# Performance work log

Hardware: AMD Instinct MI355X
Metric: run time of the kernel (lower is better)

The kernel has to match this reference:

```python
import jax, jax.numpy as jnp
import numpy as np

D_MODEL = 1024
PATCH = 16
HID = 256
VOCAB = 256

def setup_inputs() -> dict:
    key = jax.random.key(0)
    ks = jax.random.split(key, 12)
    B, N = 16, 512
    s = lambda *sh: 1.0 / np.sqrt(sh[-1])
    inp = {
        'latents': jax.random.normal(ks[0], (B, N, D_MODEL), dtype=jnp.float32),
        'target_bytes': jax.random.randint(ks[1], (B, N * PATCH), 0, VOCAB, dtype=jnp.int64),
        'W_proj': jax.random.normal(ks[2], (HID, D_MODEL), dtype=jnp.float32) * s(HID, D_MODEL),
        'b_proj': jnp.zeros((HID,), dtype=jnp.float32),
        'emb_table': jax.random.normal(ks[3], (VOCAB, HID), dtype=jnp.float32),
        'W_ih': jax.random.normal(ks[4], (3 * HID, 2 * HID), dtype=jnp.float32) * s(1, 2 * HID),
        'W_hh': jax.random.normal(ks[5], (3 * HID, HID), dtype=jnp.float32) * s(1, HID),
        'b_ih': jnp.zeros((3 * HID,), dtype=jnp.float32),
        'b_hh': jnp.zeros((3 * HID,), dtype=jnp.float32),
        'W_head': jax.random.normal(ks[6], (VOCAB, HID), dtype=jnp.float32) * s(VOCAB, HID),
        'b_head': jnp.zeros((VOCAB,), dtype=jnp.float32),
    }
    return inp

def _gru_scan(x_proj, W_hh, b_hh, h0):
    # x_proj: [T, BN, 3H] precomputed input projections (incl. b_ih)
    def step(h, xg):
        hg = h @ W_hh.T + b_hh                      # [BN, 3H]
        xr, xz, xn = jnp.split(xg, 3, axis=-1)
        hr, hz, hn = jnp.split(hg, 3, axis=-1)
        r = jax.nn.sigmoid(xr + hr)
        z = jax.nn.sigmoid(xz + hz)
        n = jnp.tanh(xn + r * hn)
        h_new = (1.0 - z) * n + z * h
        return h_new, h_new
    _, outs = jax.lax.scan(step, h0, x_proj)
    return outs                                      # [T, BN, H]

def reference(latents, target_bytes, W_proj, b_proj, emb_table, W_ih, W_hh, b_ih, b_hh, W_head, b_head):
    B, N, D = latents.shape
    BN = B * N
    latent_ctx = (latents.reshape(BN, D) @ W_proj.T + b_proj)        # [BN, H]
    targets = target_bytes.reshape(BN, PATCH)
    sos = jnp.zeros((BN, 1), dtype=targets.dtype)
    rnn_in_bytes = jnp.concatenate([sos, targets[:, :-1]], axis=1)   # [BN, P]
    emb = emb_table[rnn_in_bytes]                                    # [BN, P, H]
    lat_exp = jnp.broadcast_to(latent_ctx[:, None, :], (BN, PATCH, HID))
    rnn_input = jnp.concatenate([emb, lat_exp], axis=-1)             # [BN, P, 2H]
    x_proj = jnp.einsum('bpi,gi->bpg', rnn_input, W_ih) + b_ih       # [BN, P, 3H]
    h0 = jnp.zeros((BN, HID), dtype=latents.dtype)
    outs = _gru_scan(jnp.swapaxes(x_proj, 0, 1), W_hh, b_hh, h0)     # [P, BN, H]
    outs = jnp.swapaxes(outs, 0, 1)                                  # [BN, P, H]
    logits = jnp.einsum('bph,vh->bpv', outs, W_head) + b_head        # [BN, P, 256]
    return logits.reshape(B, N, PATCH, VOCAB)
```

## Files before the change

kernel.cpp:

```cpp
#include <hip/hip_runtime.h>
#include <math.h>

#define NSEQ 8192
#define PATCHL 16
#define HIDN 256
#define VOCABN 256

typedef __attribute__((ext_vector_type(4))) float f32x4;
typedef __attribute__((ext_vector_type(8))) short bf16x8;

__device__ __forceinline__ unsigned short f2bf(float f) {
    unsigned int x = __float_as_uint(f);
    unsigned int r = (x + 0x7fffu + ((x >> 16) & 1u)) >> 16;
    return (unsigned short)r;
}
__device__ __forceinline__ float bf2f(unsigned short b) {
    return __uint_as_float(((unsigned int)b) << 16);
}
__device__ __forceinline__ float sigf(float x)   { return 1.f / (1.f + __expf(-x)); }
__device__ __forceinline__ float tanhf_(float x) { return 2.f / (1.f + __expf(-2.f * x)) - 1.f; }

__global__ __launch_bounds__(256)
void pack_frag(const float* __restrict__ src, int ld, int col0, int nks,
               unsigned short* __restrict__ dst)
{
    const int g = blockIdx.x * 256 + threadIdx.x;
    const int lane = g & 63;
    const int ks = (g / 64) % nks;
    const int T  = g / (64 * nks);
    const float* s = src + (size_t)(T * 16 + (lane & 15)) * ld + col0 + ks * 32 + ((lane >> 4) & 3) * 8;
    unsigned int q[4];
#pragma unroll
    for (int j = 0; j < 4; j++) {
        unsigned int lo = f2bf(s[2 * j]);
        unsigned int hi = f2bf(s[2 * j + 1]);
        q[j] = lo | (hi << 16);
    }
    uint4 v; v.x = q[0]; v.y = q[1]; v.z = q[2]; v.w = q[3];
    *(uint4*)(dst + (size_t)g * 8) = v;
}

template<bool ASRC_BF16, int OUT_MODE>
__global__ __launch_bounds__(512)
void gemm_mfma(const void* __restrict__ Asrc, int lda,
               const unsigned short* __restrict__ bpack, int nks_total,
               const float* __restrict__ bias, void* __restrict__ Cdst, int ldc,
               int K)
{
    const int tid = threadIdx.x;
    const int w = tid >> 6, lane = tid & 63;
    const int l15 = lane & 15, kg = (lane >> 4) & 3;
    const int bm = blockIdx.x * 128, bn = blockIdx.y * 64;

    __shared__ unsigned short As[2][128 * 64];

    const int srow = tid >> 2;
    const int scol = (tid & 3) * 16;
    const int nkt = K / 64;

    f32x4 acc[4];
#pragma unroll
    for (int nt = 0; nt < 4; nt++) acc[nt] = 0.f;

    const int wb0 = srow * 128 + ((scol * 2) ^ ((srow & 7) << 4));
    const int wb1 = srow * 128 + ((scol * 2 + 16) ^ ((srow & 7) << 4));

#define STAGE(kt, buf) do {                                                         \
        const int gk = (kt) * 64 + scol;                                            \
        unsigned short tmp[16];                                                     \
        if (ASRC_BF16) {                                                            \
            const unsigned short* A = (const unsigned short*)Asrc;                  \
            *(uint4*)(tmp)     = *(const uint4*)(A + (size_t)(bm + srow) * lda + gk);      \
            *(uint4*)(tmp + 8) = *(const uint4*)(A + (size_t)(bm + srow) * lda + gk + 8);  \
        } else {                                                                    \
            const float* A = (const float*)Asrc;                                    \
            const float4 a0 = *(const float4*)(A + (size_t)(bm + srow) * lda + gk);       \
            const float4 a1 = *(const float4*)(A + (size_t)(bm + srow) * lda + gk + 4);   \
            const float4 a2 = *(const float4*)(A + (size_t)(bm + srow) * lda + gk + 8);   \
            const float4 a3 = *(const float4*)(A + (size_t)(bm + srow) * lda + gk + 12);  \
            tmp[0] = f2bf(a0.x);  tmp[1] = f2bf(a0.y);  tmp[2] = f2bf(a0.z);  tmp[3] = f2bf(a0.w);   \
            tmp[4] = f2bf(a1.x);  tmp[5] = f2bf(a1.y);  tmp[6] = f2bf(a1.z);  tmp[7] = f2bf(a1.w);   \
            tmp[8] = f2bf(a2.x);  tmp[9] = f2bf(a2.y);  tmp[10] = f2bf(a2.z); tmp[11] = f2bf(a2.w);  \
            tmp[12] = f2bf(a3.x); tmp[13] = f2bf(a3.y); tmp[14] = f2bf(a3.z); tmp[15] = f2bf(a3.w);  \
        }                                                                           \
        *(uint4*)((char*)As[buf] + wb0) = *(uint4*)tmp;                             \
        *(uint4*)((char*)As[buf] + wb1) = *(uint4*)(tmp + 8);                       \
    } while (0)

    STAGE(0, 0);
    __syncthreads();

    for (int kt = 0; kt < nkt; ++kt) {
        if (kt + 1 < nkt) STAGE(kt + 1, (kt + 1) & 1);
        const unsigned short* buf = As[kt & 1];
        const int row = w * 16 + l15;
#pragma unroll
        for (int ks = 0; ks < 2; ++ks) {
            const int bo = row * 128 + (((ks * 64) + kg * 16) ^ ((row & 7) << 4));
            const bf16x8 a = *(const bf16x8*)((const char*)buf + bo);
#pragma unroll
            for (int nt = 0; nt < 4; ++nt) {
                const int T = blockIdx.y * 4 + nt;
                const bf16x8 b = *(const bf16x8*)(bpack + (((size_t)T * nks_total + (kt * 2 + ks)) * 64 + lane) * 8);
                acc[nt] = __builtin_amdgcn_mfma_f32_16x16x32_bf16(a, b, acc[nt], 0, 0, 0);
            }
        }
        __syncthreads();
    }
#undef STAGE

#pragma unroll
    for (int nt = 0; nt < 4; ++nt) {
        const int n = bn + nt * 16 + l15;
        const float bv = bias ? bias[n] : 0.f;
#pragma unroll
        for (int rr = 0; rr < 4; ++rr) {
            const int m = bm + w * 16 + kg * 4 + rr;
            const float v = acc[nt][rr] + bv;
            if (OUT_MODE == 0)      ((float*)Cdst)[(size_t)m * ldc + n] = v;
            else if (OUT_MODE == 1) ((unsigned short*)Cdst)[(size_t)m * ldc + n] = f2bf(v);
            else                    ((unsigned short*)Cdst)[(size_t)m * 1024 + (n & 255) * 4 + (n >> 8)] = f2bf(v);
        }
    }
}

#define G4S 1032
__global__ __launch_bounds__(512)
__attribute__((amdgpu_waves_per_eu(2, 2)))
void gru_scan_fused(const int* __restrict__ bytes,
                    const unsigned short* __restrict__ latg4,
                    const unsigned short* __restrict__ pmx4,
                    const unsigned short* __restrict__ wpack,
                    const float* __restrict__ b_hh,
                    unsigned short* __restrict__ hh,
                    int seq0)
{
    const int tid  = threadIdx.x;
    const int w    = tid >> 6;
    const int lane = tid & 63;
    const int l15  = lane & 15;
    const int kg   = (lane >> 4) & 3;
    const int s0l  = blockIdx.x * 32;
    const int s0g  = seq0 + s0l;

    __shared__ unsigned short PMs[32 * G4S];
    __shared__ unsigned short LG[32 * G4S];
    __shared__ unsigned short H[32 * 256];
    __shared__ int BYs[512];

    BYs[tid] = bytes[(size_t)s0g * PATCHL + tid];

#pragma unroll
    for (int j = 0; j < 8; ++j) {
        const int idx = j * 512 + tid;
        const int row = idx >> 7, col = idx & 127;
        *(uint4*)(LG + row * G4S + col * 8) =
            *(const uint4*)(latg4 + (size_t)(s0g + row) * 1024 + col * 8);
    }

    float bhr[2], bhz[2], bhn[2];
#pragma unroll
    for (int nt = 0; nt < 2; nt++) {
        const int u = w * 32 + nt * 16 + l15;
        bhr[nt] = b_hh[u]; bhz[nt] = b_hh[256 + u]; bhn[nt] = b_hh[512 + u];
    }

    float hreg[2][2][4];
#pragma unroll
    for (int mt = 0; mt < 2; mt++)
#pragma unroll
        for (int nt = 0; nt < 2; nt++)
#pragma unroll
            for (int rr = 0; rr < 4; rr++) hreg[mt][nt][rr] = 0.f;

    __syncthreads();

    for (int p = 0; p < PATCHL; ++p) {
#pragma unroll
        for (int j = 0; j < 8; ++j) {
            const int idx = j * 512 + tid;
            const int row = idx >> 7, col = idx & 127;
            const int bv = p ? BYs[row * PATCHL + p - 1] : 0;
            *(uint4*)(PMs + row * G4S + col * 8) =
                *(const uint4*)(pmx4 + (size_t)bv * 1024 + col * 8);
        }

        if (p) {
#pragma unroll
            for (int rj = 0; rj < 4; ++rj) {
                const int row = w * 4 + rj;
                const int boff = (lane * 8) ^ ((row & 7) << 4);
                const ushort4 v = *(const ushort4*)((const char*)(H + row * 256) + boff);
                *(ushort4*)(hh + ((size_t)(s0l + row) * PATCHL + (p - 1)) * 256 + lane * 4) = v;
            }
        }

        f32x4 accr[2][2], accz[2][2], accn[2][2];
#pragma unroll
        for (int mt = 0; mt < 2; mt++)
#pragma unroll
            for (int nt = 0; nt < 2; nt++) {
                accr[mt][nt] = 0.f; accz[mt][nt] = 0.f; accn[mt][nt] = 0.f;
            }
        if (p != 0) {
#pragma unroll
            for (int g = 0; g < 3; ++g)
#pragma unroll
                for (int nt = 0; nt < 2; ++nt) {
                    const int T = g * 16 + w * 2 + nt;
                    bf16x8 B[8];
#pragma unroll
                    for (int ks = 0; ks < 8; ++ks)
                        B[ks] = *(const bf16x8*)(wpack + (((size_t)T * 8 + ks) * 64 + lane) * 8);
#pragma unroll
                    for (int ks = 0; ks < 8; ++ks)
#pragma unroll
                        for (int mt = 0; mt < 2; ++mt) {
                            const int s = mt * 16 + l15;
                            const int off = (ks * 64 + kg * 16) ^ ((s & 7) << 4);
                            const bf16x8 a = *(const bf16x8*)(H + s * 256 + (off >> 1));
                            if (g == 0)      accr[mt][nt] = __builtin_amdgcn_mfma_f32_16x16x32_bf16(a, B[ks], accr[mt][nt], 0, 0, 0);
                            else if (g == 1) accz[mt][nt] = __builtin_amdgcn_mfma_f32_16x16x32_bf16(a, B[ks], accz[mt][nt], 0, 0, 0);
                            else             accn[mt][nt] = __builtin_amdgcn_mfma_f32_16x16x32_bf16(a, B[ks], accn[mt][nt], 0, 0, 0);
                        }
                }
        }
        __syncthreads();

#pragma unroll
        for (int mt = 0; mt < 2; mt++)
#pragma unroll
            for (int nt = 0; nt < 2; nt++) {
                const int u = w * 32 + nt * 16 + l15;
#pragma unroll
                for (int rr = 0; rr < 4; rr++) {
                    const int sl = mt * 16 + kg * 4 + rr;
                    const ushort4 pm4 = *(const ushort4*)(PMs + sl * G4S + u * 4);
                    const ushort4 lg4 = *(const ushort4*)(LG  + sl * G4S + u * 4);
                    const float xr = bf2f(lg4.x) + bf2f(pm4.x) + bhr[nt];
                    const float xz = bf2f(lg4.y) + bf2f(pm4.y) + bhz[nt];
                    const float xn = bf2f(lg4.z) + bf2f(pm4.z);
                    const float r = sigf(xr + accr[mt][nt][rr]);
                    const float z = sigf(xz + accz[mt][nt][rr]);
                    const float n = tanhf_(xn + r * (accn[mt][nt][rr] + bhn[nt]));
                    const float hn_ = (1.f - z) * n + z * hreg[mt][nt][rr];
                    hreg[mt][nt][rr] = hn_;
                    const int bo = (2 * u) ^ ((sl & 7) << 4);
                    H[sl * 256 + (bo >> 1)] = f2bf(hn_);
                }
            }
        __syncthreads();
    }

#pragma unroll
    for (int rj = 0; rj < 4; ++rj) {
        const int row = w * 4 + rj;
        const int boff = (lane * 8) ^ ((row & 7) << 4);
        const ushort4 v = *(const ushort4*)((const char*)(H + row * 256) + boff);
        *(ushort4*)(hh + ((size_t)(s0l + row) * PATCHL + (PATCHL - 1)) * 256 + lane * 4) = v;
    }
}

extern "C" void kernel_launch(void* const* d_in, const int* in_sizes, int n_in,
                              void* d_out, int out_size, void* d_ws, size_t ws_size,
                              hipStream_t stream)
{
    const float* latents = (const float*)d_in[0];
    const int*   tb      = (const int*)d_in[1];
    const float* W_proj  = (const float*)d_in[2];
    const float* b_proj  = (const float*)d_in[3];
    const float* emb     = (const float*)d_in[4];
    const float* W_ih    = (const float*)d_in[5];
    const float* W_hh    = (const float*)d_in[6];
    const float* b_ih    = (const float*)d_in[7];
    const float* b_hh    = (const float*)d_in[8];
    const float* W_head  = (const float*)d_in[9];
    const float* b_head  = (const float*)d_in[10];
    float* out = (float*)d_out;

    char* w = (char*)d_ws;
    unsigned short* latg4   = (unsigned short*)w;          w += (size_t)NSEQ * 1024 * 2;
    unsigned short* ctxb    = (unsigned short*)w;          w += (size_t)NSEQ * HIDN * 2;
    unsigned short* pmx4    = (unsigned short*)w;          w += 256 * 1024 * 2;
    unsigned short* bpack1  = (unsigned short*)w;          w += 16 * 32 * 64 * 8 * 2;
    unsigned short* bpack2  = (unsigned short*)w;          w += 48 * 8 * 64 * 8 * 2;
    unsigned short* bpack3  = (unsigned short*)w;          w += 48 * 8 * 64 * 8 * 2;
    unsigned short* wpackG  = (unsigned short*)w;          w += 48 * 8 * 64 * 8 * 2;
    unsigned short* bpackH  = (unsigned short*)w;          w += 16 * 8 * 64 * 8 * 2;
    unsigned short* hh_c    = (unsigned short*)w;
    const size_t fixed_bytes = (size_t)(w - (char*)d_ws);
    const size_t chunk_full  = (size_t)NSEQ * PATCHL * 256 * 2;

    int nch = 1;
    while (nch < 16 && fixed_bytes + chunk_full / nch > ws_size) nch <<= 1;
    const int SPC = NSEQ / nch;

    hipLaunchKernelGGL(pack_frag, dim3(128), dim3(256), 0, stream, W_proj, 1024, 0, 32, bpack1);
    hipLaunchKernelGGL(pack_frag, dim3(96),  dim3(256), 0, stream, W_ih,   512, 256, 8, bpack2);
    hipLaunchKernelGGL(pack_frag, dim3(96),  dim3(256), 0, stream, W_ih,   512, 0,   8, bpack3);
    hipLaunchKernelGGL(pack_frag, dim3(96),  dim3(256), 0, stream, W_hh,   256, 0,   8, wpackG);
    hipLaunchKernelGGL(pack_frag, dim3(32),  dim3(256), 0, stream, W_head, 256, 0,   8, bpackH);

    hipLaunchKernelGGL((gemm_mfma<false, 2>), dim3(2, 12), dim3(512), 0, stream,
                       emb, 256, bpack3, 8, nullptr, pmx4, 1024, 256);
    hipLaunchKernelGGL((gemm_mfma<false, 1>), dim3(NSEQ / 128, 4), dim3(512), 0, stream,
                       latents, 1024, bpack1, 32, b_proj, ctxb, 256, 1024);
    hipLaunchKernelGGL((gemm_mfma<true, 2>), dim3(NSEQ / 128, 12), dim3(512), 0, stream,
                       ctxb, 256, bpack2, 8, b_ih, latg4, 1024, 256);

    for (int c = 0; c < nch; ++c) {
        const int seq0 = c * SPC;
        hipLaunchKernelGGL(gru_scan_fused, dim3(SPC / 32), dim3(512), 0, stream,
                           tb, latg4, pmx4, wpackG, b_hh, hh_c, seq0);
        hipLaunchKernelGGL((gemm_mfma<true, 0>), dim3(SPC * PATCHL / 128, 4), dim3(512), 0, stream,
                           hh_c, 256, bpackH, 8, b_head,
                           out + (size_t)seq0 * PATCHL * VOCABN, 256, 256);
    }
}
```

Baseline: 390.7 us.

## Restructure GRU scan to compute gates sequentially and load embedding projections into registers

The PMs shared-memory buffer is removed, and each thread now loads the per-step embedding-projection slices it needs straight from global memory into registers. The three gate matmuls are computed one after another with a single accumulator set, and each gate's activation is applied before the next matmul, which lowers peak register pressure. Weight fragments are loaded in smaller chunks interleaved with the MFMAs, and the forced waves_per_eu attribute is dropped. This frees about 66KB of LDS and should allow more occupancy and overlap, at the cost of more scattered small global loads for the gathered rows.

After: 349.6 us. -10.5%, faster.

```diff
diff --git a/kernel.cpp b/kernel.cpp
--- a/kernel.cpp
+++ b/kernel.cpp
@@ -126,7 +126,6 @@
 
 #define G4S 1032
 __global__ __launch_bounds__(512)
-__attribute__((amdgpu_waves_per_eu(2, 2)))
 void gru_scan_fused(const int* __restrict__ bytes,
                     const unsigned short* __restrict__ latg4,
                     const unsigned short* __restrict__ pmx4,
@@ -143,7 +142,6 @@
     const int s0l  = blockIdx.x * 32;
     const int s0g  = seq0 + s0l;
 
-    __shared__ unsigned short PMs[32 * G4S];
     __shared__ unsigned short LG[32 * G4S];
     __shared__ unsigned short H[32 * 256];
     __shared__ int BYs[512];
@@ -175,15 +173,45 @@
 
     __syncthreads();
 
+#define MFMA_GATE(gg, acc) do {                                                     \
+        _Pragma("unroll")                                                           \
+        for (int ks = 0; ks < 8; ks += 2) {                                         \
+            bf16x8 B[2][2];                                                         \
+            _Pragma("unroll")                                                       \
+            for (int dk = 0; dk < 2; ++dk)                                          \
+                _Pragma("unroll")                                                   \
+                for (int nt = 0; nt < 2; ++nt) {                                    \
+                    const int T = (gg) * 16 + w * 2 + nt;                           \
+                    B[dk][nt] = *(const bf16x8*)(wpack + (((size_t)T * 8 + ks + dk) * 64 + lane) * 8); \
+                }                                                                   \
+            _Pragma("unroll")                                                       \
+            for (int dk = 0; dk < 2; ++dk)                                          \
+                _Pragma("unroll")                                                   \
+                for (int mt = 0; mt < 2; ++mt) {                                    \
+                    const int s = mt * 16 + l15;                                    \
+                    const int off = ((ks + dk) * 64 + kg * 16) ^ ((l15 & 7) << 4);  \
+                    const bf16x8 a = *(const bf16x8*)(H + s * 256 + (off >> 1));    \
+                    _Pragma("unroll")                                               \
+                    for (int nt = 0; nt < 2; ++nt)                                  \
+                        acc[mt][nt] = __builtin_amdgcn_mfma_f32_16x16x32_bf16(a, B[dk][nt], acc[mt][nt], 0, 0, 0); \
+                }                                                                   \
+        }                                                                           \
+    } while (0)
+
     for (int p = 0; p < PATCHL; ++p) {
-#pragma unroll
-        for (int j = 0; j < 8; ++j) {
-            const int idx = j * 512 + tid;
-            const int row = idx >> 7, col = idx & 127;
-            const int bv = p ? BYs[row * PATCHL + p - 1] : 0;
-            *(uint4*)(PMs + row * G4S + col * 8) =
-                *(const uint4*)(pmx4 + (size_t)bv * 1024 + col * 8);
-        }
+        ushort4 pmreg[2][2][4];
+#pragma unroll
+        for (int mt = 0; mt < 2; mt++)
+#pragma unroll
+            for (int nt = 0; nt < 2; nt++) {
+                const int u = w * 32 + nt * 16 + l15;
+#pragma unroll
+                for (int rr = 0; rr < 4; rr++) {
+                    const int sl = mt * 16 + kg * 4 + rr;
+                    const int bv = p ? BYs[sl * PATCHL + p - 1] : 0;
+                    pmreg[mt][nt][rr] = *(const ushort4*)(pmx4 + (size_t)bv * 1024 + u * 4);
+                }
+            }
 
         if (p) {
 #pragma unroll
@@ -195,38 +223,14 @@
             }
         }
 
-        f32x4 accr[2][2], accz[2][2], accn[2][2];
-#pragma unroll
-        for (int mt = 0; mt < 2; mt++)
-#pragma unroll
-            for (int nt = 0; nt < 2; nt++) {
-                accr[mt][nt] = 0.f; accz[mt][nt] = 0.f; accn[mt][nt] = 0.f;
-            }
-        if (p != 0) {
-#pragma unroll
-            for (int g = 0; g < 3; ++g)
-#pragma unroll
-                for (int nt = 0; nt < 2; ++nt) {
-                    const int T = g * 16 + w * 2 + nt;
-                    bf16x8 B[8];
-#pragma unroll
-                    for (int ks = 0; ks < 8; ++ks)
-                        B[ks] = *(const bf16x8*)(wpack + (((size_t)T * 8 + ks) * 64 + lane) * 8);
-#pragma unroll
-                    for (int ks = 0; ks < 8; ++ks)
-#pragma unroll
-                        for (int mt = 0; mt < 2; ++mt) {
-                            const int s = mt * 16 + l15;
-                            const int off = (ks * 64 + kg * 16) ^ ((s & 7) << 4);
-                            const bf16x8 a = *(const bf16x8*)(H + s * 256 + (off >> 1));
-                            if (g == 0)      accr[mt][nt] = __builtin_amdgcn_mfma_f32_16x16x32_bf16(a, B[ks], accr[mt][nt], 0, 0, 0);
-                            else if (g == 1) accz[mt][nt] = __builtin_amdgcn_mfma_f32_16x16x32_bf16(a, B[ks], accz[mt][nt], 0, 0, 0);
-                            else             accn[mt][nt] = __builtin_amdgcn_mfma_f32_16x16x32_bf16(a, B[ks], accn[mt][nt], 0, 0, 0);
-                        }
-                }
-        }
-        __syncthreads();
-
+        f32x4 acc[2][2];
+#pragma unroll
+        for (int mt = 0; mt < 2; mt++)
+#pragma unroll
+            for (int nt = 0; nt < 2; nt++) acc[mt][nt] = 0.f;
+        if (p) MFMA_GATE(0, acc);
+
+        float rv[2][2][4], xz[2][2][4], xn[2][2][4];
 #pragma unroll
         for (int mt = 0; mt < 2; mt++)
 #pragma unroll
@@ -235,15 +239,48 @@
 #pragma unroll
                 for (int rr = 0; rr < 4; rr++) {
                     const int sl = mt * 16 + kg * 4 + rr;
-                    const ushort4 pm4 = *(const ushort4*)(PMs + sl * G4S + u * 4);
-                    const ushort4 lg4 = *(const ushort4*)(LG  + sl * G4S + u * 4);
+                    const ushort4 lg4 = *(const ushort4*)(LG + sl * G4S + u * 4);
+                    const ushort4 pm4 = pmreg[mt][nt][rr];
                     const float xr = bf2f(lg4.x) + bf2f(pm4.x) + bhr[nt];
-                    const float xz = bf2f(lg4.y) + bf2f(pm4.y) + bhz[nt];
-                    const float xn = bf2f(lg4.z) + bf2f(pm4.z);
-                    const float r = sigf(xr + accr[mt][nt][rr]);
-                    const float z = sigf(xz + accz[mt][nt][rr]);
-                    const float n = tanhf_(xn + r * (accn[mt][nt][rr] + bhn[nt]));
-                    const float hn_ = (1.f - z) * n + z * hreg[mt][nt][rr];
+                    rv[mt][nt][rr] = sigf(xr + acc[mt][nt][rr]);
+                    xz[mt][nt][rr] = bf2f(lg4.y) + bf2f(pm4.y) + bhz[nt];
+                    xn[mt][nt][rr] = bf2f(lg4.z) + bf2f(pm4.z);
+                }
+            }
+
+#pragma unroll
+        for (int mt = 0; mt < 2; mt++)
+#pragma unroll
+            for (int nt = 0; nt < 2; nt++) acc[mt][nt] = 0.f;
+        if (p) MFMA_GATE(1, acc);
+
+        float zv[2][2][4];
+#pragma unroll
+        for (int mt = 0; mt < 2; mt++)
+#pragma unroll
+            for (int nt = 0; nt < 2; nt++)
+#pragma unroll
+                for (int rr = 0; rr < 4; rr++)
+                    zv[mt][nt][rr] = sigf(xz[mt][nt][rr] + acc[mt][nt][rr]);
+
+#pragma unroll
+        for (int mt = 0; mt < 2; mt++)
+#pragma unroll
+            for (int nt = 0; nt < 2; nt++) acc[mt][nt] = 0.f;
+        if (p) MFMA_GATE(2, acc);
+
+        __syncthreads();
+
+#pragma unroll
+        for (int mt = 0; mt < 2; mt++)
+#pragma unroll
+            for (int nt = 0; nt < 2; nt++) {
+                const int u = w * 32 + nt * 16 + l15;
+#pragma unroll
+                for (int rr = 0; rr < 4; rr++) {
+                    const int sl = mt * 16 + kg * 4 + rr;
+                    const float n = tanhf_(xn[mt][nt][rr] + rv[mt][nt][rr] * (acc[mt][nt][rr] + bhn[nt]));
+                    const float hn_ = (1.f - zv[mt][nt][rr]) * n + zv[mt][nt][rr] * hreg[mt][nt][rr];
                     hreg[mt][nt][rr] = hn_;
                     const int bo = (2 * u) ^ ((sl & 7) << 4);
                     H[sl * 256 + (bo >> 1)] = f2bf(hn_);
@@ -251,6 +288,7 @@
             }
         __syncthreads();
     }
+#undef MFMA_GATE
 
 #pragma unroll
     for (int rj = 0; rj < 4; ++rj) {
```
